# Optimization experiments

Measured on AMD Instinct MI355X. Metric: run time of the kernel, lower is better.

## Reference

```python
import jax, jax.numpy as jnp
import numpy as np

EPSILON = 0.1        # SinkhornConfig.epsilon
NUM_INNER_ITER = 10  # SinkhornConfig.num_inner_iter
STAB = 1e-8          # denominator stabilizer from forward()


def setup_inputs() -> dict:
    key = jax.random.key(0)
    k1, k2 = jax.random.split(key)
    source_features = jax.random.uniform(k1, (8192, 64), dtype=jnp.float32)
    target_features = jax.random.uniform(k2, (8192, 64), dtype=jnp.float32)
    return {"source_features": source_features, "target_features": target_features}


def _cost_matrix(s, t):
    # pairwise Euclidean distance ||s_i - t_j||_2, computed without the
    # [Ns, Nt, D] broadcast the torch code materializes (same math).
    s2 = jnp.sum(s * s, axis=1, keepdims=True)          # [Ns, 1]
    t2 = jnp.sum(t * t, axis=1, keepdims=True).T        # [1, Nt]
    sq = s2 + t2 - 2.0 * (s @ t.T)                      # [Ns, Nt]
    return jnp.sqrt(jnp.maximum(sq, 0.0))


def reference(source_features, target_features):
    ns = source_features.shape[0]
    nt = target_features.shape[0]
    # uniform weights, normalized (source_weights/target_weights is None path)
    sw = jnp.full((ns, 1), 1.0 / ns, dtype=source_features.dtype)
    tw = jnp.full((nt, 1), 1.0 / nt, dtype=target_features.dtype)

    cost = _cost_matrix(source_features, target_features)   # [Ns, Nt]
    kernel = jnp.exp(-cost / EPSILON)                        # Gibbs kernel

    u = jnp.ones((ns, 1), dtype=cost.dtype)
    v = jnp.ones((nt, 1), dtype=cost.dtype)
    for _ in range(NUM_INNER_ITER):  # fixed small trip count
        u = sw / (kernel @ v + STAB)
        v = tw / (kernel.T @ u + STAB)

    coupling = u * kernel * v.T                              # [Ns, Nt]
    sinkhorn_dist = jnp.sum(coupling * cost) / (ns * nt)     # reduction='mean'
    return sinkhorn_dist, coupling, u, v
```

## Files before the change

kernel.cpp:

```cpp
#include <hip/hip_runtime.h>
#include <hip/hip_bf16.h>
#include <math.h>

#define NSRC 8192
#define NTGT 8192
#define DIM 64

__device__ __forceinline__ float wave_reduce_sum(float x) {
#pragma unroll
  for (int off = 32; off > 0; off >>= 1) x += __shfl_down(x, off, 64);
  return x;
}

__device__ __forceinline__ float bflo(unsigned int u) {
  return __uint_as_float(u << 16);
}
__device__ __forceinline__ float bfhi(unsigned int u) {
  return __uint_as_float(u & 0xFFFF0000u);
}

__global__ __launch_bounds__(256) void norms_k(const float* __restrict__ S,
                                               const float* __restrict__ T,
                                               float* __restrict__ s2,
                                               float* __restrict__ t2) {
  int i = blockIdx.x * 256 + threadIdx.x;
  if (i >= NSRC + NTGT) return;
  const float* base = (i < NSRC) ? (S + (size_t)i * DIM)
                                 : (T + (size_t)(i - NSRC) * DIM);
  const float4* p = (const float4*)base;
  float a = 0.f;
#pragma unroll
  for (int k = 0; k < DIM / 4; ++k) {
    float4 v = p[k];
    a += v.x * v.x + v.y * v.y + v.z * v.z + v.w * v.w;
  }
  if (i < NSRC) s2[i] = a;
  else          t2[i - NSRC] = a;
}

__global__ __launch_bounds__(256) void init_k(float* __restrict__ c,
                                              float* __restrict__ v_out) {
  int i = blockIdx.x * 256 + threadIdx.x;
  if (i < NTGT) {
    c[i] = 0.f;
    v_out[i] = 1.f;
  }
}

#define BM 64
#define BN 128
__global__ __launch_bounds__(256) void kbuild_k(const float* __restrict__ S,
                                                const float* __restrict__ T,
                                                const float* __restrict__ s2,
                                                const float* __restrict__ t2,
                                                float* __restrict__ Kf,
                                                __hip_bfloat16* __restrict__ Kb,
                                                __hip_bfloat16* __restrict__ KbT) {
  __shared__ __align__(16) char smem[52224];
  float (*sT)[68] = (float (*)[68])smem;
  float (*tT)[68] = (float (*)[68])(smem + 17408);
  unsigned short (*tr)[72] = (unsigned short (*)[72])smem;

  const int bn = blockIdx.x * BN;
  const int bm = blockIdx.y * BM;
  const int tid = threadIdx.x;

  {
    const float4* sg = (const float4*)(S + (size_t)bm * DIM);
#pragma unroll
    for (int k = 0; k < 4; ++k) {
      int f = tid + 256 * k;
      int row = f >> 4, c4 = f & 15;
      *(float4*)&sT[row][c4 * 4] = sg[f];
    }
    const float4* tg = (const float4*)(T + (size_t)bn * DIM);
#pragma unroll
    for (int k = 0; k < 8; ++k) {
      int f = tid + 256 * k;
      int row = f >> 4, c4 = f & 15;
      *(float4*)&tT[row][c4 * 4] = tg[f];
    }
  }
  __syncthreads();

  const int tx = tid & 15;
  const int ty = tid >> 4;

  float acc[4][8];
#pragma unroll
  for (int a = 0; a < 4; ++a)
#pragma unroll
    for (int b = 0; b < 8; ++b) acc[a][b] = 0.f;

  for (int k = 0; k < DIM; k += 4) {
    float4 sr[4], trg[8];
#pragma unroll
    for (int a = 0; a < 4; ++a) sr[a] = *(float4*)&sT[ty + 16 * a][k];
#pragma unroll
    for (int b = 0; b < 8; ++b) trg[b] = *(float4*)&tT[tx + 16 * b][k];
#pragma unroll
    for (int a = 0; a < 4; ++a)
#pragma unroll
      for (int b = 0; b < 8; ++b) {
        acc[a][b] += sr[a].x * trg[b].x;
        acc[a][b] += sr[a].y * trg[b].y;
        acc[a][b] += sr[a].z * trg[b].z;
        acc[a][b] += sr[a].w * trg[b].w;
      }
  }
  __syncthreads();

  float s2r[4];
#pragma unroll
  for (int a = 0; a < 4; ++a) s2r[a] = s2[bm + ty + 16 * a];

#pragma unroll
  for (int a = 0; a < 4; ++a) {
    int gi = bm + ty + 16 * a;
#pragma unroll
    for (int b = 0; b < 8; ++b) {
      int gj = bn + tx + 16 * b;
      float sq = s2r[a] + t2[gj] - 2.f * acc[a][b];
      float cost = sqrtf(fmaxf(sq, 0.f));
      float kv = __expf(-10.f * cost);
      size_t off = (size_t)gi * NTGT + gj;
      __hip_bfloat16 kb = __float2bfloat16(kv);
      if (Kf) Kf[off] = kv;
      if (Kb) Kb[off] = kb;
      if (KbT) tr[tx + 16 * b][ty + 16 * a] = __hip_bfloat16_raw(kb).x;
    }
  }

  if (KbT) {
    __syncthreads();
    int r = tid >> 1, seg = tid & 1;
    const uint4* src = (const uint4*)&tr[r][seg * 32];
    uint4 d0 = src[0], d1 = src[1], d2 = src[2], d3 = src[3];
    uint4* dst = (uint4*)(KbT + (size_t)(bn + r) * NSRC + bm + seg * 32);
    dst[0] = d0; dst[1] = d1; dst[2] = d2; dst[3] = d3;
  }
}

__global__ __launch_bounds__(256) void rowsum_k(const unsigned short* __restrict__ P,
                                                const float* __restrict__ x,
                                                float* __restrict__ y) {
  int row = blockIdx.x * 4 + (threadIdx.x >> 6);
  int lane = threadIdx.x & 63;
  const uint4* r4 = (const uint4*)(P + (size_t)row * NTGT);
  const float4* x4 = (const float4*)x;
  float a = 0.f;
#pragma unroll 4
  for (int s = lane; s < NTGT / 8; s += 64) {
    uint4 q = r4[s];
    float4 xa = x4[2 * s], xb = x4[2 * s + 1];
    a += bflo(q.x) * xa.x + bfhi(q.x) * xa.y
       + bflo(q.y) * xa.z + bfhi(q.y) * xa.w
       + bflo(q.z) * xb.x + bfhi(q.z) * xb.y
       + bflo(q.w) * xb.z + bfhi(q.w) * xb.w;
  }
  a = wave_reduce_sum(a);
  if (lane == 0) y[row] = (1.0f / 8192.0f) / (a + 1e-8f);
}

__global__ __launch_bounds__(256) void coupling_bf16_k(
    const unsigned short* __restrict__ Kb,
    const float* __restrict__ u,
    const float* __restrict__ v,
    float* __restrict__ C,
    float* __restrict__ partials) {
  __shared__ float red[4];
  size_t g = (size_t)blockIdx.x * 256 + threadIdx.x;
  size_t base = g * 32;
  int i = (int)(base >> 13);
  int j0 = (int)(base & 8191);
  float ui = u[i];
  const uint4* kp = (const uint4*)(Kb + base);
  const float4* vp = (const float4*)(v + j0);
  float part = 0.f;
#pragma unroll
  for (int s = 0; s < 4; ++s) {
    uint4 q = kp[s];
    float4 va = vp[2 * s], vb = vp[2 * s + 1];
    float k0 = bflo(q.x), k1 = bfhi(q.x), k2 = bflo(q.y), k3 = bfhi(q.y);
    float k4 = bflo(q.z), k5 = bfhi(q.z), k6 = bflo(q.w), k7 = bfhi(q.w);
    float c0 = ui * k0 * va.x, c1 = ui * k1 * va.y;
    float c2 = ui * k2 * va.z, c3 = ui * k3 * va.w;
    float c4 = ui * k4 * vb.x, c5 = ui * k5 * vb.y;
    float c6 = ui * k6 * vb.z, c7 = ui * k7 * vb.w;
    part += c0 * __logf(fmaxf(k0, 1e-37f)) + c1 * __logf(fmaxf(k1, 1e-37f)) +
            c2 * __logf(fmaxf(k2, 1e-37f)) + c3 * __logf(fmaxf(k3, 1e-37f)) +
            c4 * __logf(fmaxf(k4, 1e-37f)) + c5 * __logf(fmaxf(k5, 1e-37f)) +
            c6 * __logf(fmaxf(k6, 1e-37f)) + c7 * __logf(fmaxf(k7, 1e-37f));
    float* cw = C + base + 8 * s;
    *(float4*)cw       = make_float4(c0, c1, c2, c3);
    *(float4*)(cw + 4) = make_float4(c4, c5, c6, c7);
  }
  part = wave_reduce_sum(part);
  int wid = threadIdx.x >> 6, lane = threadIdx.x & 63;
  if (lane == 0) red[wid] = part;
  __syncthreads();
  if (threadIdx.x == 0)
    partials[blockIdx.x] = red[0] + red[1] + red[2] + red[3];
}

__global__ __launch_bounds__(256) void rowsum_f32_k(const float* __restrict__ K,
                                                    const float* __restrict__ v,
                                                    float* __restrict__ u_out) {
  int row = (blockIdx.x * 256 + threadIdx.x) >> 6;
  int lane = threadIdx.x & 63;
  const float4* r4 = (const float4*)(K + (size_t)row * NTGT);
  const float4* v4 = (const float4*)v;
  float a = 0.f;
#pragma unroll 4
  for (int j = lane; j < NTGT / 4; j += 64) {
    float4 k4 = r4[j];
    float4 vv = v4[j];
    a += k4.x * vv.x + k4.y * vv.y + k4.z * vv.z + k4.w * vv.w;
  }
  a = wave_reduce_sum(a);
  if (lane == 0) u_out[row] = (1.0f / NSRC) / (a + 1e-8f);
}

__global__ __launch_bounds__(256) void colsum_f32_k(const float* __restrict__ K,
                                                    const float* __restrict__ u,
                                                    float* __restrict__ c) {
  int j = blockIdx.x * 1024 + threadIdx.x * 4;
  int i0 = blockIdx.y * 64;
  float a0 = 0.f, a1 = 0.f, a2 = 0.f, a3 = 0.f;
#pragma unroll 8
  for (int i = i0; i < i0 + 64; ++i) {
    float ui = u[i];
    float4 k4 = *(const float4*)(K + (size_t)i * NTGT + j);
    a0 += k4.x * ui; a1 += k4.y * ui; a2 += k4.z * ui; a3 += k4.w * ui;
  }
  atomicAdd(&c[j + 0], a0);
  atomicAdd(&c[j + 1], a1);
  atomicAdd(&c[j + 2], a2);
  atomicAdd(&c[j + 3], a3);
}

__global__ __launch_bounds__(256) void finishv_k(float* __restrict__ c,
                                                 float* __restrict__ v_out) {
  int j = blockIdx.x * 256 + threadIdx.x;
  v_out[j] = (1.0f / NTGT) / (c[j] + 1e-8f);
  c[j] = 0.f;
}

__global__ __launch_bounds__(256) void coupling_f32_k(float* __restrict__ K,
                                                      const float* __restrict__ u,
                                                      const float* __restrict__ v,
                                                      float* __restrict__ partials) {
  __shared__ float red[4];
  size_t t0 = (size_t)blockIdx.x * 2048 + threadIdx.x;
  float part = 0.f;
#pragma unroll
  for (int s = 0; s < 8; ++s) {
    size_t f4 = t0 + (size_t)s * 256;
    size_t base = f4 * 4;
    int i = (int)(base >> 13);
    int j = (int)(base & 8191);
    float4 k4 = *(float4*)(K + base);
    float ui = u[i];
    float4 vv = *(const float4*)(v + j);
    float c0 = ui * k4.x * vv.x;
    float c1 = ui * k4.y * vv.y;
    float c2 = ui * k4.z * vv.z;
    float c3 = ui * k4.w * vv.w;
    part += c0 * __logf(k4.x) + c1 * __logf(k4.y) +
            c2 * __logf(k4.z) + c3 * __logf(k4.w);
    *(float4*)(K + base) = make_float4(c0, c1, c2, c3);
  }
  part = wave_reduce_sum(part);
  int wid = threadIdx.x >> 6, lane = threadIdx.x & 63;
  if (lane == 0) red[wid] = part;
  __syncthreads();
  if (threadIdx.x == 0)
    partials[blockIdx.x] = red[0] + red[1] + red[2] + red[3];
}

__global__ __launch_bounds__(256) void finalize_k(const float* __restrict__ partials,
                                                  float* __restrict__ out) {
  __shared__ float red[4];
  float a = 0.f;
  for (int i = threadIdx.x; i < 8192; i += 256) a += partials[i];
  a = wave_reduce_sum(a);
  int wid = threadIdx.x >> 6, lane = threadIdx.x & 63;
  if (lane == 0) red[wid] = a;
  __syncthreads();
  if (threadIdx.x == 0)
    out[0] = (red[0] + red[1] + red[2] + red[3]) *
             (-0.1f / ((float)NSRC * (float)NTGT));
}

extern "C" void kernel_launch(void* const* d_in, const int* in_sizes, int n_in,
                              void* d_out, int out_size, void* d_ws, size_t ws_size,
                              hipStream_t stream) {
  const float* S = (const float*)d_in[0];
  const float* T = (const float*)d_in[1];
  float* out = (float*)d_out;

  float* C  = out + 1;
  float* u  = out + 1 + (size_t)NSRC * NTGT;
  float* vv = u + NSRC;

  __hip_bfloat16* KbT = (__hip_bfloat16*)C;

  char* wsb = (char*)d_ws;
  float* s2       = (float*)(wsb);
  float* t2       = (float*)(wsb + (32 << 10));
  float* partials = (float*)(wsb + (64 << 10));
  float* c        = (float*)(wsb + (96 << 10));
  const size_t KB_OFF = 512 << 10;
  const size_t KB_BYTES = (size_t)NSRC * NTGT * 2;
  __hip_bfloat16* Kb = (__hip_bfloat16*)(wsb + KB_OFF);

  bool full = ws_size >= KB_OFF + KB_BYTES;

  norms_k<<<(NSRC + NTGT + 255) / 256, 256, 0, stream>>>(S, T, s2, t2);
  init_k<<<NTGT / 256, 256, 0, stream>>>(c, vv);

  if (full) {
    kbuild_k<<<dim3(NTGT / BN, NSRC / BM), 256, 0, stream>>>(
        S, T, s2, t2, nullptr, Kb, KbT);
    for (int it = 0; it < 10; ++it) {
      rowsum_k<<<NSRC / 4, 256, 0, stream>>>((const unsigned short*)Kb, vv, u);
      rowsum_k<<<NTGT / 4, 256, 0, stream>>>((const unsigned short*)KbT, u, vv);
    }
    coupling_bf16_k<<<8192, 256, 0, stream>>>(
        (const unsigned short*)Kb, u, vv, C, partials);
  } else {
    kbuild_k<<<dim3(NTGT / BN, NSRC / BM), 256, 0, stream>>>(
        S, T, s2, t2, C, nullptr, nullptr);
    for (int it = 0; it < 10; ++it) {
      rowsum_f32_k<<<NSRC * 64 / 256, 256, 0, stream>>>(C, vv, u);
      colsum_f32_k<<<dim3(8, 128), 256, 0, stream>>>(C, u, c);
      finishv_k<<<NTGT / 256, 256, 0, stream>>>(c, vv);
    }
    coupling_f32_k<<<8192, 256, 0, stream>>>(C, u, vv, partials);
  }
  finalize_k<<<1, 256, 0, stream>>>(partials, out);
}
```

Measured before the change: 778.4 us.

## Build Gibbs kernel with split-bf16 MFMA and fuse first row-sum into build

Replaces the scalar FP32 distance GEMM in the kernel-build step with bf16 MFMA 32x32x16 instructions. A hi/lo split of the inputs (three products) keeps close to FP32 accuracy, and a prep kernel writes the split operands. The build kernel also accumulates the row sums of the bf16 kernel through atomics, so the first u update comes from those sums and one full-matrix row-sum pass is skipped. The transposed copy is now written through a shared staging tile. Costs are an extra prep launch, atomic contention, and possible small accuracy differences from the split-bf16 product and the atomic summation order.

```diff
diff --git a/kernel.cpp b/kernel.cpp
--- a/kernel.cpp
+++ b/kernel.cpp
@@ -6,6 +6,9 @@
 #define NTGT 8192
 #define DIM 64
 
+typedef short bf16x8 __attribute__((ext_vector_type(8)));
+typedef float f32x16 __attribute__((ext_vector_type(16)));
+
 __device__ __forceinline__ float wave_reduce_sum(float x) {
 #pragma unroll
   for (int off = 32; off > 0; off >>= 1) x += __shfl_down(x, off, 64);
@@ -17,6 +20,10 @@
 }
 __device__ __forceinline__ float bfhi(unsigned int u) {
   return __uint_as_float(u & 0xFFFF0000u);
+}
+__device__ __forceinline__ unsigned short f2bfr(float x) {
+  __hip_bfloat16 b = __float2bfloat16(x);
+  return __hip_bfloat16_raw(b).x;
 }
 
 __global__ __launch_bounds__(256) void norms_k(const float* __restrict__ S,
@@ -38,107 +45,145 @@
   else          t2[i - NSRC] = a;
 }
 
+__global__ __launch_bounds__(256) void prep_k(const float* __restrict__ S,
+                                              const float* __restrict__ T,
+                                              unsigned short* __restrict__ Shi,
+                                              unsigned short* __restrict__ Slo,
+                                              unsigned short* __restrict__ Thi,
+                                              unsigned short* __restrict__ Tlo) {
+  int i = blockIdx.x * 256 + threadIdx.x;
+  const float* src;
+  unsigned short *dh, *dl;
+  if (i < 65536) { src = S; dh = Shi; dl = Slo; }
+  else { src = T; dh = Thi; dl = Tlo; i -= 65536; }
+  const float4* p = (const float4*)(src + (size_t)i * 8);
+  float4 x = p[0], y = p[1];
+  float vals[8] = {x.x, x.y, x.z, x.w, y.x, y.y, y.z, y.w};
+  unsigned int h[8], lo[8];
+#pragma unroll
+  for (int e = 0; e < 8; ++e) {
+    unsigned short hr = f2bfr(vals[e]);
+    h[e] = hr;
+    lo[e] = f2bfr(vals[e] - bflo(hr));
+  }
+  uint4 hw = make_uint4(h[0] | (h[1] << 16), h[2] | (h[3] << 16),
+                        h[4] | (h[5] << 16), h[6] | (h[7] << 16));
+  uint4 lw = make_uint4(lo[0] | (lo[1] << 16), lo[2] | (lo[3] << 16),
+                        lo[4] | (lo[5] << 16), lo[6] | (lo[7] << 16));
+  *(uint4*)(dh + (size_t)i * 8) = hw;
+  *(uint4*)(dl + (size_t)i * 8) = lw;
+}
+
 __global__ __launch_bounds__(256) void init_k(float* __restrict__ c,
-                                              float* __restrict__ v_out) {
+                                              float* __restrict__ v_out,
+                                              float* __restrict__ rowacc) {
   int i = blockIdx.x * 256 + threadIdx.x;
   if (i < NTGT) {
     c[i] = 0.f;
     v_out[i] = 1.f;
-  }
-}
-
-#define BM 64
-#define BN 128
-__global__ __launch_bounds__(256) void kbuild_k(const float* __restrict__ S,
-                                                const float* __restrict__ T,
-                                                const float* __restrict__ s2,
-                                                const float* __restrict__ t2,
-                                                float* __restrict__ Kf,
-                                                __hip_bfloat16* __restrict__ Kb,
-                                                __hip_bfloat16* __restrict__ KbT) {
-  __shared__ __align__(16) char smem[52224];
-  float (*sT)[68] = (float (*)[68])smem;
-  float (*tT)[68] = (float (*)[68])(smem + 17408);
-  unsigned short (*tr)[72] = (unsigned short (*)[72])smem;
-
-  const int bn = blockIdx.x * BN;
-  const int bm = blockIdx.y * BM;
+    rowacc[i] = 0.f;
+  }
+}
+
+#define PR(r) ((((r) >> 3) + (((r)&7) << 3)))
+
+__global__ __launch_bounds__(256) void kbuild_mfma_k(
+    const unsigned short* __restrict__ Shi, const unsigned short* __restrict__ Slo,
+    const unsigned short* __restrict__ Thi, const unsigned short* __restrict__ Tlo,
+    const float* __restrict__ s2, const float* __restrict__ t2,
+    __hip_bfloat16* __restrict__ Kb, __hip_bfloat16* __restrict__ KbT,
+    float* __restrict__ rowacc) {
+  __shared__ unsigned short sAh[64][72], sAl[64][72];
+  __shared__ unsigned short sBh[64][72], sBl[64][72];
+  __shared__ unsigned short stage[64][72];
+  __shared__ float sS2[64], sT2[64];
+
   const int tid = threadIdx.x;
+  const int bm = blockIdx.y * 64, bn = blockIdx.x * 64;
+
+#pragma unroll
+  for (int p = 0; p < 2; ++p) {
+    int f = tid + 256 * p;
+    int row = f >> 3, seg = (f & 7) * 8;
+    *(uint4*)&sAh[row][seg] = ((const uint4*)(Shi + (size_t)bm * DIM))[f];
+    *(uint4*)&sAl[row][seg] = ((const uint4*)(Slo + (size_t)bm * DIM))[f];
+    *(uint4*)&sBh[row][seg] = ((const uint4*)(Thi + (size_t)bn * DIM))[f];
+    *(uint4*)&sBl[row][seg] = ((const uint4*)(Tlo + (size_t)bn * DIM))[f];
+  }
+  if (tid < 64) sS2[tid] = s2[bm + tid];
+  else if (tid < 128) sT2[tid - 64] = t2[bn + (tid - 64)];
+  __syncthreads();
+
+  const int w = tid >> 6, l = tid & 63;
+  const int wr = w >> 1, wc = w & 1;
+  const int arow = 32 * wr + (l & 31);
+  const int brow = 32 * wc + (l & 31);
+  const int kh = 8 * (l >> 5);
+
+  f32x16 acc;
+#pragma unroll
+  for (int i = 0; i < 16; ++i) acc[i] = 0.f;
+
+#pragma unroll
+  for (int ks = 0; ks < 4; ++ks) {
+    int ko = 16 * ks + kh;
+    bf16x8 ah = *(const bf16x8*)&sAh[arow][ko];
+    bf16x8 al = *(const bf16x8*)&sAl[arow][ko];
+    bf16x8 bh = *(const bf16x8*)&sBh[brow][ko];
+    bf16x8 bl = *(const bf16x8*)&sBl[brow][ko];
+    acc = __builtin_amdgcn_mfma_f32_32x32x16_bf16(ah, bh, acc, 0, 0, 0);
+    acc = __builtin_amdgcn_mfma_f32_32x32x16_bf16(ah, bl, acc, 0, 0, 0);
+    acc = __builtin_amdgcn_mfma_f32_32x32x16_bf16(al, bh, acc, 0, 0, 0);
+  }
+
+#pragma unroll
+  for (int j = 0; j < 16; ++j) {
+    int rl = (j & 3) + 8 * (j >> 2) + 4 * (l >> 5);
+    int row = 32 * wr + rl, col = 32 * wc + (l & 31);
+    float sq = sS2[row] + sT2[col] - 2.f * acc[j];
+    float kv = __expf(-10.f * sqrtf(fmaxf(sq, 0.f)));
+    stage[PR(row)][col] = f2bfr(kv);
+  }
+  __syncthreads();
 
   {
-    const float4* sg = (const float4*)(S + (size_t)bm * DIM);
-#pragma unroll
-    for (int k = 0; k < 4; ++k) {
-      int f = tid + 256 * k;
-      int row = f >> 4, c4 = f & 15;
-      *(float4*)&sT[row][c4 * 4] = sg[f];
-    }
-    const float4* tg = (const float4*)(T + (size_t)bn * DIM);
-#pragma unroll
-    for (int k = 0; k < 8; ++k) {
-      int f = tid + 256 * k;
-      int row = f >> 4, c4 = f & 15;
-      *(float4*)&tT[row][c4 * 4] = tg[f];
-    }
-  }
-  __syncthreads();
-
-  const int tx = tid & 15;
-  const int ty = tid >> 4;
-
-  float acc[4][8];
-#pragma unroll
-  for (int a = 0; a < 4; ++a)
-#pragma unroll
-    for (int b = 0; b < 8; ++b) acc[a][b] = 0.f;
-
-  for (int k = 0; k < DIM; k += 4) {
-    float4 sr[4], trg[8];
-#pragma unroll
-    for (int a = 0; a < 4; ++a) sr[a] = *(float4*)&sT[ty + 16 * a][k];
-#pragma unroll
-    for (int b = 0; b < 8; ++b) trg[b] = *(float4*)&tT[tx + 16 * b][k];
-#pragma unroll
-    for (int a = 0; a < 4; ++a)
-#pragma unroll
-      for (int b = 0; b < 8; ++b) {
-        acc[a][b] += sr[a].x * trg[b].x;
-        acc[a][b] += sr[a].y * trg[b].y;
-        acc[a][b] += sr[a].z * trg[b].z;
-        acc[a][b] += sr[a].w * trg[b].w;
-      }
-  }
-  __syncthreads();
-
-  float s2r[4];
-#pragma unroll
-  for (int a = 0; a < 4; ++a) s2r[a] = s2[bm + ty + 16 * a];
-
-#pragma unroll
-  for (int a = 0; a < 4; ++a) {
-    int gi = bm + ty + 16 * a;
-#pragma unroll
-    for (int b = 0; b < 8; ++b) {
-      int gj = bn + tx + 16 * b;
-      float sq = s2r[a] + t2[gj] - 2.f * acc[a][b];
-      float cost = sqrtf(fmaxf(sq, 0.f));
-      float kv = __expf(-10.f * cost);
-      size_t off = (size_t)gi * NTGT + gj;
-      __hip_bfloat16 kb = __float2bfloat16(kv);
-      if (Kf) Kf[off] = kv;
-      if (Kb) Kb[off] = kb;
-      if (KbT) tr[tx + 16 * b][ty + 16 * a] = __hip_bfloat16_raw(kb).x;
-    }
-  }
-
-  if (KbT) {
-    __syncthreads();
-    int r = tid >> 1, seg = tid & 1;
-    const uint4* src = (const uint4*)&tr[r][seg * 32];
-    uint4 d0 = src[0], d1 = src[1], d2 = src[2], d3 = src[3];
-    uint4* dst = (uint4*)(KbT + (size_t)(bn + r) * NSRC + bm + seg * 32);
-    dst[0] = d0; dst[1] = d1; dst[2] = d2; dst[3] = d3;
-  }
+    int row = tid >> 2, q = tid & 3;
+    float a = 0.f;
+#pragma unroll
+    for (int m = 0; m < 16; ++m)
+      a += bflo((unsigned int)stage[PR(row)][16 * q + m]);
+    a += __shfl_down(a, 1, 4);
+    a += __shfl_down(a, 2, 4);
+    if (q == 0) atomicAdd(&rowacc[bm + row], a);
+  }
+
+#pragma unroll
+  for (int p = 0; p < 2; ++p) {
+    int f = tid + 256 * p;
+    int row = f >> 3, seg = (f & 7) * 8;
+    *(uint4*)(Kb + (size_t)(bm + row) * NTGT + bn + seg) =
+        *(const uint4*)&stage[PR(row)][seg];
+  }
+#pragma unroll
+  for (int p = 0; p < 2; ++p) {
+    int f = tid + 256 * p;
+    int tcol = f >> 3, gro = f & 7;
+    unsigned int wds[4];
+#pragma unroll
+    for (int e = 0; e < 4; ++e) {
+      unsigned int a0 = stage[gro + 8 * (2 * e)][tcol];
+      unsigned int a1 = stage[gro + 8 * (2 * e + 1)][tcol];
+      wds[e] = a0 | (a1 << 16);
+    }
+    *(uint4*)(KbT + (size_t)(bn + tcol) * NSRC + bm + 8 * gro) =
+        make_uint4(wds[0], wds[1], wds[2], wds[3]);
+  }
+}
+
+__global__ __launch_bounds__(256) void initu_k(const float* __restrict__ rowacc,
+                                               float* __restrict__ u) {
+  int i = blockIdx.x * 256 + threadIdx.x;
+  u[i] = (1.0f / NSRC) / (rowacc[i] + 1e-8f);
 }
 
 __global__ __launch_bounds__(256) void rowsum_k(const unsigned short* __restrict__ P,
@@ -203,6 +248,72 @@
     partials[blockIdx.x] = red[0] + red[1] + red[2] + red[3];
 }
 
+#define BM 64
+#define BN 128
+__global__ __launch_bounds__(256) void kbuild_k(const float* __restrict__ S,
+                                                const float* __restrict__ T,
+                                                const float* __restrict__ s2,
+                                                const float* __restrict__ t2,
+                                                float* __restrict__ Kf) {
+  __shared__ float sT[BM][68];
+  __shared__ float tT[BN][68];
+  const int bn = blockIdx.x * BN;
+  const int bm = blockIdx.y * BM;
+  const int tid = threadIdx.x;
+  {
+    const float4* sg = (const float4*)(S + (size_t)bm * DIM);
+#pragma unroll
+    for (int k = 0; k < 4; ++k) {
+      int f = tid + 256 * k;
+      int row = f >> 4, c4 = f & 15;
+      *(float4*)&sT[row][c4 * 4] = sg[f];
+    }
+    const float4* tg = (const float4*)(T + (size_t)bn * DIM);
+#pragma unroll
+    for (int k = 0; k < 8; ++k) {
+      int f = tid + 256 * k;
+      int row = f >> 4, c4 = f & 15;
+      *(float4*)&tT[row][c4 * 4] = tg[f];
+    }
+  }
+  __syncthreads();
+  const int tx = tid & 15;
+  const int ty = tid >> 4;
+  float acc[4][8];
+#pragma unroll
+  for (int a = 0; a < 4; ++a)
+#pragma unroll
+    for (int b = 0; b < 8; ++b) acc[a][b] = 0.f;
+  for (int k = 0; k < DIM; k += 4) {
+    float4 sr[4], trg[8];
+#pragma unroll
+    for (int a = 0; a < 4; ++a) sr[a] = *(float4*)&sT[ty + 16 * a][k];
+#pragma unroll
+    for (int b = 0; b < 8; ++b) trg[b] = *(float4*)&tT[tx + 16 * b][k];
+#pragma unroll
+    for (int a = 0; a < 4; ++a)
+#pragma unroll
+      for (int b = 0; b < 8; ++b) {
+        acc[a][b] += sr[a].x * trg[b].x;
+        acc[a][b] += sr[a].y * trg[b].y;
+        acc[a][b] += sr[a].z * trg[b].z;
+        acc[a][b] += sr[a].w * trg[b].w;
+      }
+  }
+#pragma unroll
+  for (int a = 0; a < 4; ++a) {
+    int gi = bm + ty + 16 * a;
+    float s2v = s2[gi];
+#pragma unroll
+    for (int b = 0; b < 8; ++b) {
+      int gj = bn + tx + 16 * b;
+      float sq = s2v + t2[gj] - 2.f * acc[a][b];
+      float cost = sqrtf(fmaxf(sq, 0.f));
+      Kf[(size_t)gi * NTGT + gj] = __expf(-10.f * cost);
+    }
+  }
+}
+
 __global__ __launch_bounds__(256) void rowsum_f32_k(const float* __restrict__ K,
                                                     const float* __restrict__ v,
                                                     float* __restrict__ u_out) {
@@ -310,27 +421,35 @@
   float* t2       = (float*)(wsb + (32 << 10));
   float* partials = (float*)(wsb + (64 << 10));
   float* c        = (float*)(wsb + (96 << 10));
-  const size_t KB_OFF = 512 << 10;
+  float* rowacc   = (float*)(wsb + (128 << 10));
+  unsigned short* Shi = (unsigned short*)(wsb + (1 << 20));
+  unsigned short* Slo = (unsigned short*)(wsb + (2 << 20));
+  unsigned short* Thi = (unsigned short*)(wsb + (3 << 20));
+  unsigned short* Tlo = (unsigned short*)(wsb + (4 << 20));
+  const size_t KB_OFF = (size_t)8 << 20;
   const size_t KB_BYTES = (size_t)NSRC * NTGT * 2;
   __hip_bfloat16* Kb = (__hip_bfloat16*)(wsb + KB_OFF);
 
   bool full = ws_size >= KB_OFF + KB_BYTES;
 
   norms_k<<<(NSRC + NTGT + 255) / 256, 256, 0, stream>>>(S, T, s2, t2);
-  init_k<<<NTGT / 256, 256, 0, stream>>>(c, vv);
 
   if (full) {
-    kbuild_k<<<dim3(NTGT / BN, NSRC / BM), 256, 0, stream>>>(
-        S, T, s2, t2, nullptr, Kb, KbT);
+    prep_k<<<512, 256, 0, stream>>>(S, T, Shi, Slo, Thi, Tlo);
+    init_k<<<NTGT / 256, 256, 0, stream>>>(c, vv, rowacc);
+    kbuild_mfma_k<<<dim3(128, 128), 256, 0, stream>>>(
+        Shi, Slo, Thi, Tlo, s2, t2, Kb, KbT, rowacc);
+    initu_k<<<NSRC / 256, 256, 0, stream>>>(rowacc, u);
     for (int it = 0; it < 10; ++it) {
-      rowsum_k<<<NSRC / 4, 256, 0, stream>>>((const unsigned short*)Kb, vv, u);
+      if (it > 0)
+        rowsum_k<<<NSRC / 4, 256, 0, stream>>>((const unsigned short*)Kb, vv, u);
       rowsum_k<<<NTGT / 4, 256, 0, stream>>>((const unsigned short*)KbT, u, vv);
     }
     coupling_bf16_k<<<8192, 256, 0, stream>>>(
         (const unsigned short*)Kb, u, vv, C, partials);
   } else {
-    kbuild_k<<<dim3(NTGT / BN, NSRC / BM), 256, 0, stream>>>(
-        S, T, s2, t2, C, nullptr, nullptr);
+    init_k<<<NTGT / 256, 256, 0, stream>>>(c, vv, partials );
+    kbuild_k<<<dim3(NTGT / BN, NSRC / BM), 256, 0, stream>>>(S, T, s2, t2, C);
     for (int it = 0; it < 10; ++it) {
       rowsum_f32_k<<<NSRC * 64 / 256, 256, 0, stream>>>(C, vv, u);
       colsum_f32_k<<<dim3(8, 128), 256, 0, stream>>>(C, u, c);
```

After: 686.2 us. -11.9%, faster.
